# Optimization experiments

Hardware: AMD Instinct MI355X
Metric: run time of the kernel (lower is better)

The kernel has to match this reference:

```python
import jax, jax.numpy as jnp
import numpy as np

N, C, H, W = 16, 256, 48, 96
S = 64   # num_s = 2*num_state_mid; also num_n = mids*mids = 64 (must match)
EPS = 1e-5


def setup_inputs() -> dict:
    key = jax.random.key(0)
    ks = jax.random.split(key, 11)
    sc = 0.05
    return {
        "x": jax.random.normal(ks[0], (N, C, H, W), jnp.float32),
        "edge": jax.random.normal(ks[1], (N, 2, H, W), jnp.float32),
        # conv_state: Conv2d(C, S, 1) with bias
        "Ws": jax.random.normal(ks[2], (S, C), jnp.float32) * sc,
        "bs": jax.random.normal(ks[3], (S,), jnp.float32) * sc,
        # conv_proj: Conv2d(C, S, 1) with bias
        "Wp": jax.random.normal(ks[4], (S, C), jnp.float32) * sc,
        "bp": jax.random.normal(ks[5], (S,), jnp.float32) * sc,
        # GCN conv1: Conv1d(num_n, num_n, 1, bias=False)
        "W1": jax.random.normal(ks[6], (S, S), jnp.float32) * sc,
        # GCN conv2: Conv1d(S, S, 1, bias=False)
        "W2": jax.random.normal(ks[7], (S, S), jnp.float32) * sc,
        # conv_extend: Conv2d(S, C, 1, bias=False)
        "We": jax.random.normal(ks[8], (C, S), jnp.float32) * sc,
        # BatchNorm2d(C) affine params (training-mode batch stats used in forward)
        "gamma": jnp.ones((C,), jnp.float32),
        "beta": jnp.zeros((C,), jnp.float32),
    }


def reference(x, edge, Ws, bs, Wp, bp, W1, W2, We, gamma, beta):
    n, c, h, w = x.shape
    s = Ws.shape[0]
    # edge softmax over channels, take class-1 probability map  -> (n,1,h,w)
    edge_g = jax.nn.softmax(edge, axis=1)[:, 1:2]

    # 1x1 convs as channel matmuls
    xs = jnp.einsum('oc,nchw->nohw', Ws, x) + bs[None, :, None, None]
    xs = xs.reshape(n, s, h * w)                        # (n,S,HW)
    xp = jnp.einsum('oc,nchw->nohw', Wp, x) + bp[None, :, None, None]
    # x_proj_region + x_proj_edge == xp * (1 + edge_gate)
    comb = (xp * (1.0 + edge_g)).reshape(n, s, h * w)
    comb = jax.nn.softmax(comb, axis=-1)                # softmax over spatial

    # project to graph space: (n,S,HW) @ (n,HW,S) -> (n,S,S)
    xn = jnp.einsum('nsk,ntk->nst', xs, comb)

    # GCN: conv1 over node dim (last axis mixes via W1), subtract, conv2 over state dim, relu
    hh = jnp.einsum('ij,nsj->nsi', W1, xn) - xn
    hh = jax.nn.relu(jnp.einsum('ij,njk->nik', W2, hh))

    # back-project: (n,S,S) @ (n,S,HW) -> (n,S,HW) -> (n,S,H,W)
    xr = jnp.einsum('nst,ntk->nsk', hh, comb).reshape(n, s, h, w)

    # conv_extend (no bias) then BatchNorm2d in training mode (biased batch var)
    ext = jnp.einsum('os,nshw->nohw', We, xr)
    mean = ext.mean(axis=(0, 2, 3), keepdims=True)
    var = ext.var(axis=(0, 2, 3), keepdims=True)
    bn = gamma[None, :, None, None] * (ext - mean) * jax.lax.rsqrt(var + EPS) \
         + beta[None, :, None, None]
    return x + bn
```

## Files before the change

### kernel.cpp

```cpp
#include <hip/hip_runtime.h>

#define HW 4608
#define NB 16
#define CC 256
#define SS 64
#define EPS 1e-5f
#define NSPLIT 24

typedef __attribute__((ext_vector_type(8))) short short8;
typedef __attribute__((ext_vector_type(4))) float f32x4;

__device__ __forceinline__ ushort f2bf(float f) {
    uint u = __float_as_uint(f);
    return (ushort)((u + 0x7FFFu + ((u >> 16) & 1u)) >> 16);
}
__device__ __forceinline__ float bf2f(ushort h) {
    return __uint_as_float(((uint)h) << 16);
}

__global__ __launch_bounds__(256) void k_wf(const float* __restrict__ Ws,
                                            const float* __restrict__ Wp,
                                            ushort* __restrict__ Wf) {
    int idx = blockIdx.x * 256 + threadIdx.x;
    int j = idx & 7, r = (idx >> 3) & 127, kq = (idx >> 10) & 3, cs = idx >> 12;
    int c = cs * 32 + kq * 8 + j;
    float v = (r < 64) ? Ws[r * CC + c] : Wp[(r - 64) * CC + c];
    Wf[idx] = f2bf(v);
}

__global__ __launch_bounds__(256) void k_proj(const float* __restrict__ x,
                                              const ushort* __restrict__ Wf,
                                              const float* __restrict__ bs,
                                              const float* __restrict__ bp,
                                              const float* __restrict__ edge,
                                              ushort* __restrict__ xsb,
                                              ushort* __restrict__ Eb,
                                              float* __restrict__ rsum) {
    __shared__ __align__(16) ushort Bl[4 * 128 * 8];
    int n = blockIdx.y, k0 = blockIdx.x * 128;
    int tid = threadIdx.x, lane = tid & 63, w = tid >> 6;
    int wr = w >> 1, wn = w & 1;
    int q = lane >> 4, li = lane & 15;
    int sn = tid & 127, kq0 = (tid >> 7) * 2;
    f32x4 acc[4][4] = {};
    for (int cs = 0; cs < 8; cs++) {
#pragma unroll
        for (int kk = 0; kk < 2; kk++) {
            int kq = kq0 + kk;
            union { ushort u[8]; uint4 v; } tmp;
#pragma unroll
            for (int j = 0; j < 8; j++) {
                float vv = x[((size_t)n * CC + cs * 32 + kq * 8 + j) * HW + k0 + sn];
                tmp.u[j] = f2bf(vv);
            }
            *(uint4*)&Bl[(kq * 128 + sn) * 8] = tmp.v;
        }
        __syncthreads();
        short8 af[4], bfr[4];
#pragma unroll
        for (int m = 0; m < 4; m++) {
            int r = wr * 64 + m * 16 + li;
            uint4 t = *(const uint4*)&Wf[((cs * 4 + q) * 128 + r) * 8];
            af[m] = *(short8*)&t;
        }
#pragma unroll
        for (int nn = 0; nn < 4; nn++) {
            int nl = wn * 64 + nn * 16 + li;
            uint4 t = *(const uint4*)&Bl[(q * 128 + nl) * 8];
            bfr[nn] = *(short8*)&t;
        }
#pragma unroll
        for (int m = 0; m < 4; m++)
#pragma unroll
            for (int nn = 0; nn < 4; nn++)
                acc[m][nn] = __builtin_amdgcn_mfma_f32_16x16x32_bf16(af[m], bfr[nn], acc[m][nn], 0, 0, 0);
        __syncthreads();
    }
    if (wr == 0) {
#pragma unroll
        for (int m = 0; m < 4; m++) {
#pragma unroll
            for (int rr = 0; rr < 4; rr++) {
                int s = m * 16 + q * 4 + rr;
                float bv = bs[s];
#pragma unroll
                for (int nn = 0; nn < 4; nn++) {
                    int col = k0 + wn * 64 + nn * 16 + li;
                    xsb[((size_t)n * SS + s) * HW + col] = f2bf(acc[m][nn][rr] + bv);
                }
            }
        }
    } else {
        float ga[4];
#pragma unroll
        for (int nn = 0; nn < 4; nn++) {
            int col = k0 + wn * 64 + nn * 16 + li;
            float e0 = edge[((size_t)n * 2 + 0) * HW + col];
            float e1 = edge[((size_t)n * 2 + 1) * HW + col];
            ga[nn] = 1.f + 1.f / (1.f + __expf(e0 - e1));
        }
        float rp[4][4];
#pragma unroll
        for (int m = 0; m < 4; m++) {
#pragma unroll
            for (int rr = 0; rr < 4; rr++) {
                int s = m * 16 + q * 4 + rr;
                float bv = bp[s];
                float sum = 0.f;
#pragma unroll
                for (int nn = 0; nn < 4; nn++) {
                    int col = k0 + wn * 64 + nn * 16 + li;
                    float e = __expf((acc[m][nn][rr] + bv) * ga[nn]);
                    sum += e;
                    Eb[((size_t)n * SS + s) * HW + col] = f2bf(e);
                }
                rp[m][rr] = sum;
            }
        }
#pragma unroll
        for (int b = 1; b < 16; b <<= 1)
#pragma unroll
            for (int m = 0; m < 4; m++)
#pragma unroll
                for (int rr = 0; rr < 4; rr++)
                    rp[m][rr] += __shfl_xor(rp[m][rr], b, 64);
        if (li == 0) {
#pragma unroll
            for (int m = 0; m < 4; m++)
#pragma unroll
                for (int rr = 0; rr < 4; rr++)
                    atomicAdd(&rsum[n * SS + m * 16 + q * 4 + rr], rp[m][rr]);
        }
    }
}

__global__ __launch_bounds__(256) void k_graph(const ushort* __restrict__ xsb,
                                               const ushort* __restrict__ Eb,
                                               float* __restrict__ Up,
                                               float* __restrict__ Pp) {
    int n = blockIdx.y, sp = blockIdx.x;
    int kbase = sp * (HW / NSPLIT);
    int tid = threadIdx.x, lane = tid & 63, w = tid >> 6;
    int q = lane >> 4, li = lane & 15;
    bool isP = w >= 2;
    int half = w & 1;
    const ushort* Arow = isP ? Eb : xsb;
    f32x4 acc[2][4] = {};
    for (int ks = 0; ks < (HW / NSPLIT) / 32; ks++) {
        int kb = kbase + ks * 32 + q * 8;
        short8 af[2], bfr[4];
#pragma unroll
        for (int mt = 0; mt < 2; mt++) {
            int s = half * 32 + mt * 16 + li;
            uint4 t = *(const uint4*)&Arow[((size_t)n * SS + s) * HW + kb];
            af[mt] = *(short8*)&t;
        }
#pragma unroll
        for (int nt = 0; nt < 4; nt++) {
            int tt = nt * 16 + li;
            uint4 t = *(const uint4*)&Eb[((size_t)n * SS + tt) * HW + kb];
            bfr[nt] = *(short8*)&t;
        }
#pragma unroll
        for (int mt = 0; mt < 2; mt++)
#pragma unroll
            for (int nt = 0; nt < 4; nt++)
                acc[mt][nt] = __builtin_amdgcn_mfma_f32_16x16x32_bf16(af[mt], bfr[nt], acc[mt][nt], 0, 0, 0);
    }
    float* dst = (isP ? Pp : Up) + ((size_t)sp * NB + n) * 4096;
#pragma unroll
    for (int mt = 0; mt < 2; mt++)
#pragma unroll
        for (int nt = 0; nt < 4; nt++)
#pragma unroll
            for (int rr = 0; rr < 4; rr++) {
                int row = half * 32 + mt * 16 + q * 4 + rr;
                int col = nt * 16 + li;
                dst[row * 64 + col] = acc[mt][nt][rr];
            }
}

__global__ __launch_bounds__(256) void k_red(const float* __restrict__ Up,
                                             const float* __restrict__ Pp,
                                             float* __restrict__ U,
                                             float* __restrict__ P) {
    int idx = blockIdx.x * 256 + threadIdx.x;
    const float* src = (idx < 65536) ? Up : Pp;
    float* dst = (idx < 65536) ? U : P;
    int o = idx & 65535;
    float s = 0.f;
    for (int sp = 0; sp < NSPLIT; sp++) s += src[(size_t)sp * 65536 + o];
    dst[o] = s;
}

__global__ __launch_bounds__(256) void k_gcn(const float* __restrict__ U,
                                             const float* __restrict__ rsum,
                                             const float* __restrict__ W1,
                                             const float* __restrict__ W2,
                                             const float* __restrict__ We,
                                             float* __restrict__ M,
                                             ushort* __restrict__ Mf) {
    __shared__ __align__(16) float A[64 * 68];
    __shared__ __align__(16) float B[64 * 68];
    __shared__ __align__(16) float Cb[64 * 68];
    __shared__ float rs[64];
    int n = blockIdx.x;
    int cc = blockIdx.y;
    int tid = threadIdx.x;
    int t0 = tid >> 4, t1 = tid & 15;
    if (tid < 64) rs[tid] = 1.0f / rsum[n * SS + tid];
    __syncthreads();
#pragma unroll
    for (int i = 0; i < 16; i++) {
        int idx = tid + i * 256;
        int r = idx >> 6, cth = idx & 63;
        A[cth * 68 + r] = U[n * 4096 + idx] * rs[cth];
        B[cth * 68 + r] = W1[idx];
    }
    __syncthreads();
    {
        float acc[4][4] = {};
        for (int j = 0; j < 64; j++) {
            float4 a4 = *(const float4*)&A[j * 68 + t0 * 4];
            float4 b4 = *(const float4*)&B[j * 68 + t1 * 4];
            float a[4] = {a4.x, a4.y, a4.z, a4.w};
            float b[4] = {b4.x, b4.y, b4.z, b4.w};
#pragma unroll
            for (int p = 0; p < 4; p++)
#pragma unroll
                for (int qq = 0; qq < 4; qq++) acc[p][qq] += a[p] * b[qq];
        }
#pragma unroll
        for (int p = 0; p < 4; p++)
#pragma unroll
            for (int qq = 0; qq < 4; qq++) {
                acc[p][qq] -= A[(t1 * 4 + qq) * 68 + (t0 * 4 + p)];
                Cb[(t0 * 4 + p) * 68 + t1 * 4 + qq] = acc[p][qq];
            }
    }
    __syncthreads();
#pragma unroll
    for (int i = 0; i < 16; i++) {
        int idx = tid + i * 256;
        int r = idx >> 6, cth = idx & 63;
        B[cth * 68 + r] = W2[idx];
    }
    __syncthreads();
    {
        float acc[4][4] = {};
        for (int j = 0; j < 64; j++) {
            float4 a4 = *(const float4*)&B[j * 68 + t0 * 4];
            float4 b4 = *(const float4*)&Cb[j * 68 + t1 * 4];
            float a[4] = {a4.x, a4.y, a4.z, a4.w};
            float b[4] = {b4.x, b4.y, b4.z, b4.w};
#pragma unroll
            for (int p = 0; p < 4; p++)
#pragma unroll
                for (int qq = 0; qq < 4; qq++) acc[p][qq] += a[p] * b[qq];
        }
        __syncthreads();
#pragma unroll
        for (int p = 0; p < 4; p++)
#pragma unroll
            for (int qq = 0; qq < 4; qq++)
                A[(t0 * 4 + p) * 68 + t1 * 4 + qq] = fmaxf(acc[p][qq], 0.f);
    }
    __syncthreads();
#pragma unroll
    for (int i = 0; i < 16; i++) {
        int idx = tid + i * 256;
        int c = idx >> 6, j = idx & 63;
        B[j * 68 + c] = We[(cc * 64 + c) * 64 + j];
    }
    __syncthreads();
    {
        float acc[4][4] = {};
        for (int j = 0; j < 64; j++) {
            float4 a4 = *(const float4*)&B[j * 68 + t0 * 4];
            float4 b4 = *(const float4*)&A[j * 68 + t1 * 4];
            float a[4] = {a4.x, a4.y, a4.z, a4.w};
            float b[4] = {b4.x, b4.y, b4.z, b4.w};
#pragma unroll
            for (int p = 0; p < 4; p++)
#pragma unroll
                for (int qq = 0; qq < 4; qq++) acc[p][qq] += a[p] * b[qq];
        }
#pragma unroll
        for (int p = 0; p < 4; p++) {
            int c = cc * 64 + t0 * 4 + p;
            float v[4];
#pragma unroll
            for (int qq = 0; qq < 4; qq++) v[qq] = acc[p][qq] * rs[t1 * 4 + qq];
            float4 st = {v[0], v[1], v[2], v[3]};
            *(float4*)&M[((size_t)n * CC + c) * 64 + t1 * 4] = st;
#pragma unroll
            for (int qq = 0; qq < 4; qq++) {
                int t = t1 * 4 + qq;
                Mf[(size_t)n * 16384 + ((t >> 3) * 256 + c) * 8 + (t & 7)] = f2bf(v[qq]);
            }
        }
    }
}

__global__ __launch_bounds__(256) void k_stats(const float* __restrict__ M,
                                               const float* __restrict__ P,
                                               const float* __restrict__ rsum,
                                               const float* __restrict__ gamma,
                                               const float* __restrict__ beta,
                                               float* __restrict__ sc,
                                               float* __restrict__ bi) {
    __shared__ float ms[64];
    __shared__ float rst[64];
    __shared__ float red[256];
    int c = blockIdx.x;
    int tid = threadIdx.x;
    float qa = 0.f, sa = 0.f;
    for (int n = 0; n < NB; n++) {
        if (tid < 64) ms[tid] = M[((size_t)n * CC + c) * 64 + tid];
        else if (tid < 128) rst[tid - 64] = rsum[n * SS + tid - 64];
        __syncthreads();
#pragma unroll
        for (int p = 0; p < 16; p++) {
            int e = p * 256 + tid;
            qa += ms[e >> 6] * ms[e & 63] * P[n * 4096 + e];
        }
        if ((tid & 63) == 0) {
#pragma unroll
            for (int p = 0; p < 16; p++) {
                int s = (p * 256 + tid) >> 6;
                sa += ms[s] * rst[s];
            }
        }
        __syncthreads();
    }
    red[tid] = qa;
    __syncthreads();
    for (int off = 128; off > 0; off >>= 1) {
        if (tid < off) red[tid] += red[tid + off];
        __syncthreads();
    }
    float qtot = red[0];
    __syncthreads();
    red[tid] = sa;
    __syncthreads();
    for (int off = 128; off > 0; off >>= 1) {
        if (tid < off) red[tid] += red[tid + off];
        __syncthreads();
    }
    float stot = red[0];
    if (tid == 0) {
        const float invM = 1.0f / ((float)NB * (float)HW);
        float mean = stot * invM;
        float var = qtot * invM - mean * mean;
        float s = gamma[c] * rsqrtf(var + EPS);
        sc[c] = s;
        bi[c] = beta[c] - s * mean;
    }
}

__global__ __launch_bounds__(256) void k_out(const float* __restrict__ x,
                                             const ushort* __restrict__ Mf,
                                             const ushort* __restrict__ Eb,
                                             const float* __restrict__ sc,
                                             const float* __restrict__ bi,
                                             float* __restrict__ out) {
    __shared__ __align__(16) ushort Bl[8 * 64 * 8];
    int n = blockIdx.y, k0 = blockIdx.x * 64;
    int tid = threadIdx.x, lane = tid & 63, w = tid >> 6;
    int q = lane >> 4, li = lane & 15;
    {
        int nl = tid & 63, pr = tid >> 6;
#pragma unroll
        for (int kk = 0; kk < 2; kk++) {
            int kq = pr * 2 + kk;
            union { ushort u[8]; uint4 v; } tmp;
#pragma unroll
            for (int j = 0; j < 8; j++)
                tmp.u[j] = Eb[((size_t)n * SS + kq * 8 + j) * HW + k0 + nl];
            *(uint4*)&Bl[(kq * 64 + nl) * 8] = tmp.v;
        }
    }
    __syncthreads();
    f32x4 acc[4][4] = {};
#pragma unroll
    for (int ks = 0; ks < 2; ks++) {
        short8 af[4], bfr[4];
#pragma unroll
        for (int mt = 0; mt < 4; mt++) {
            int c = w * 64 + mt * 16 + li;
            uint4 t = *(const uint4*)&Mf[(size_t)n * 16384 + ((ks * 4 + q) * 256 + c) * 8];
            af[mt] = *(short8*)&t;
        }
#pragma unroll
        for (int nt = 0; nt < 4; nt++) {
            int nl = nt * 16 + li;
            uint4 t = *(const uint4*)&Bl[((ks * 4 + q) * 64 + nl) * 8];
            bfr[nt] = *(short8*)&t;
        }
#pragma unroll
        for (int mt = 0; mt < 4; mt++)
#pragma unroll
            for (int nt = 0; nt < 4; nt++)
                acc[mt][nt] = __builtin_amdgcn_mfma_f32_16x16x32_bf16(af[mt], bfr[nt], acc[mt][nt], 0, 0, 0);
    }
#pragma unroll
    for (int mt = 0; mt < 4; mt++) {
#pragma unroll
        for (int rr = 0; rr < 4; rr++) {
            int c = w * 64 + mt * 16 + q * 4 + rr;
            float s_ = sc[c], bv = bi[c];
            size_t base = ((size_t)n * CC + c) * HW + k0;
#pragma unroll
            for (int nt = 0; nt < 4; nt++) {
                int col = nt * 16 + li;
                out[base + col] = x[base + col] + s_ * acc[mt][nt][rr] + bv;
            }
        }
    }
}

extern "C" void kernel_launch(void* const* d_in, const int* in_sizes, int n_in,
                              void* d_out, int out_size, void* d_ws, size_t ws_size,
                              hipStream_t stream) {
    const float* x = (const float*)d_in[0];
    const float* edge = (const float*)d_in[1];
    const float* Ws = (const float*)d_in[2];
    const float* bs = (const float*)d_in[3];
    const float* Wp = (const float*)d_in[4];
    const float* bp = (const float*)d_in[5];
    const float* W1 = (const float*)d_in[6];
    const float* W2 = (const float*)d_in[7];
    const float* We = (const float*)d_in[8];
    const float* gamma = (const float*)d_in[9];
    const float* beta = (const float*)d_in[10];
    float* out = (float*)d_out;

    char* base = (char*)d_ws;
    ushort* Wf  = (ushort*)base;                    base += 65536;
    ushort* xsb = (ushort*)base;                    base += 9437184;
    ushort* Eb  = (ushort*)base;                    base += 9437184;
    float*  Up  = (float*)base;                     base += (size_t)NSPLIT * NB * 4096 * 4;
    float*  Pp  = (float*)base;                     base += (size_t)NSPLIT * NB * 4096 * 4;
    float*  U   = (float*)base;                     base += 262144;
    float*  P   = (float*)base;                     base += 262144;
    float*  rsum= (float*)base;                     base += 4096;
    float*  M   = (float*)base;                     base += 1048576;
    ushort* Mf  = (ushort*)base;                    base += 524288;
    float*  sc  = (float*)base;                     base += 1024;
    float*  bi  = (float*)base;                     base += 1024;

    hipMemsetAsync(rsum, 0, 1024 * sizeof(float), stream);
    k_wf<<<128, 256, 0, stream>>>(Ws, Wp, Wf);
    k_proj<<<dim3(36, NB), 256, 0, stream>>>(x, Wf, bs, bp, edge, xsb, Eb, rsum);
    k_graph<<<dim3(NSPLIT, NB), 256, 0, stream>>>(xsb, Eb, Up, Pp);
    k_red<<<512, 256, 0, stream>>>(Up, Pp, U, P);
    k_gcn<<<dim3(NB, 4), 256, 0, stream>>>(U, rsum, W1, W2, We, M, Mf);
    k_stats<<<256, 256, 0, stream>>>(M, P, rsum, gamma, beta, sc, bi);
    k_out<<<dim3(72, NB), 256, 0, stream>>>(x, Mf, Eb, sc, bi, out);
}
```

Before: 235.8 us.

## Register double-buffer loads in projection and graph kernels, drop LDS staging

k_proj now loads x straight from global into registers, one column per lane, instead of staging through shared memory with two barriers per step. The next channel slice and weight fragment are prefetched while the current MFMAs run. Tile width is halved to 64 columns so the grid doubles. k_graph gets the same register double-buffered prefetch, and k_out batches its x loads ahead of the stores. The trade-off is higher register pressure and column-strided global loads that may coalesce less well.

```diff
diff --git a/kernel.cpp b/kernel.cpp
--- a/kernel.cpp
+++ b/kernel.cpp
@@ -36,46 +36,59 @@
                                               ushort* __restrict__ xsb,
                                               ushort* __restrict__ Eb,
                                               float* __restrict__ rsum) {
-    __shared__ __align__(16) ushort Bl[4 * 128 * 8];
-    int n = blockIdx.y, k0 = blockIdx.x * 128;
+    int n = blockIdx.y, k0 = blockIdx.x * 64;
     int tid = threadIdx.x, lane = tid & 63, w = tid >> 6;
     int wr = w >> 1, wn = w & 1;
     int q = lane >> 4, li = lane & 15;
-    int sn = tid & 127, kq0 = (tid >> 7) * 2;
-    f32x4 acc[4][4] = {};
+    const float* xb = x + (size_t)n * CC * HW + k0 + wn * 32 + li;
+
+    float pfB[2][2][8];
+    short8 af[2][4];
+    f32x4 acc[4][2] = {};
+
+#pragma unroll
+    for (int nt = 0; nt < 2; nt++)
+#pragma unroll
+        for (int j = 0; j < 8; j++)
+            pfB[0][nt][j] = xb[(size_t)(q * 8 + j) * HW + nt * 16];
+#pragma unroll
+    for (int m = 0; m < 4; m++) {
+        int r = wr * 64 + m * 16 + li;
+        uint4 t = *(const uint4*)&Wf[((0 * 4 + q) * 128 + r) * 8];
+        af[0][m] = *(short8*)&t;
+    }
+
+#pragma unroll
     for (int cs = 0; cs < 8; cs++) {
-#pragma unroll
-        for (int kk = 0; kk < 2; kk++) {
-            int kq = kq0 + kk;
-            union { ushort u[8]; uint4 v; } tmp;
-#pragma unroll
-            for (int j = 0; j < 8; j++) {
-                float vv = x[((size_t)n * CC + cs * 32 + kq * 8 + j) * HW + k0 + sn];
-                tmp.u[j] = f2bf(vv);
-            }
-            *(uint4*)&Bl[(kq * 128 + sn) * 8] = tmp.v;
-        }
-        __syncthreads();
-        short8 af[4], bfr[4];
-#pragma unroll
-        for (int m = 0; m < 4; m++) {
-            int r = wr * 64 + m * 16 + li;
-            uint4 t = *(const uint4*)&Wf[((cs * 4 + q) * 128 + r) * 8];
-            af[m] = *(short8*)&t;
-        }
-#pragma unroll
-        for (int nn = 0; nn < 4; nn++) {
-            int nl = wn * 64 + nn * 16 + li;
-            uint4 t = *(const uint4*)&Bl[(q * 128 + nl) * 8];
-            bfr[nn] = *(short8*)&t;
+        int cur = cs & 1, nxt = cur ^ 1;
+        if (cs < 7) {
+#pragma unroll
+            for (int nt = 0; nt < 2; nt++)
+#pragma unroll
+                for (int j = 0; j < 8; j++)
+                    pfB[nxt][nt][j] = xb[(size_t)((cs + 1) * 32 + q * 8 + j) * HW + nt * 16];
+#pragma unroll
+            for (int m = 0; m < 4; m++) {
+                int r = wr * 64 + m * 16 + li;
+                uint4 t = *(const uint4*)&Wf[(((cs + 1) * 4 + q) * 128 + r) * 8];
+                af[nxt][m] = *(short8*)&t;
+            }
+        }
+        short8 bfr[2];
+#pragma unroll
+        for (int nt = 0; nt < 2; nt++) {
+            union { ushort u[8]; short8 s; } tmp;
+#pragma unroll
+            for (int j = 0; j < 8; j++) tmp.u[j] = f2bf(pfB[cur][nt][j]);
+            bfr[nt] = tmp.s;
         }
 #pragma unroll
         for (int m = 0; m < 4; m++)
 #pragma unroll
-            for (int nn = 0; nn < 4; nn++)
-                acc[m][nn] = __builtin_amdgcn_mfma_f32_16x16x32_bf16(af[m], bfr[nn], acc[m][nn], 0, 0, 0);
-        __syncthreads();
-    }
+            for (int nt = 0; nt < 2; nt++)
+                acc[m][nt] = __builtin_amdgcn_mfma_f32_16x16x32_bf16(af[cur][m], bfr[nt], acc[m][nt], 0, 0, 0);
+    }
+
     if (wr == 0) {
 #pragma unroll
         for (int m = 0; m < 4; m++) {
@@ -84,20 +97,20 @@
                 int s = m * 16 + q * 4 + rr;
                 float bv = bs[s];
 #pragma unroll
-                for (int nn = 0; nn < 4; nn++) {
-                    int col = k0 + wn * 64 + nn * 16 + li;
-                    xsb[((size_t)n * SS + s) * HW + col] = f2bf(acc[m][nn][rr] + bv);
+                for (int nt = 0; nt < 2; nt++) {
+                    int col = k0 + wn * 32 + nt * 16 + li;
+                    xsb[((size_t)n * SS + s) * HW + col] = f2bf(acc[m][nt][rr] + bv);
                 }
             }
         }
     } else {
-        float ga[4];
-#pragma unroll
-        for (int nn = 0; nn < 4; nn++) {
-            int col = k0 + wn * 64 + nn * 16 + li;
+        float ga[2];
+#pragma unroll
+        for (int nt = 0; nt < 2; nt++) {
+            int col = k0 + wn * 32 + nt * 16 + li;
             float e0 = edge[((size_t)n * 2 + 0) * HW + col];
             float e1 = edge[((size_t)n * 2 + 1) * HW + col];
-            ga[nn] = 1.f + 1.f / (1.f + __expf(e0 - e1));
+            ga[nt] = 1.f + 1.f / (1.f + __expf(e0 - e1));
         }
         float rp[4][4];
 #pragma unroll
@@ -108,9 +121,9 @@
                 float bv = bp[s];
                 float sum = 0.f;
 #pragma unroll
-                for (int nn = 0; nn < 4; nn++) {
-                    int col = k0 + wn * 64 + nn * 16 + li;
-                    float e = __expf((acc[m][nn][rr] + bv) * ga[nn]);
+                for (int nt = 0; nt < 2; nt++) {
+                    int col = k0 + wn * 32 + nt * 16 + li;
+                    float e = __expf((acc[m][nt][rr] + bv) * ga[nt]);
                     sum += e;
                     Eb[((size_t)n * SS + s) * HW + col] = f2bf(e);
                 }
@@ -145,27 +158,47 @@
     bool isP = w >= 2;
     int half = w & 1;
     const ushort* Arow = isP ? Eb : xsb;
+    const int NITER = (HW / NSPLIT) / 32;
     f32x4 acc[2][4] = {};
-    for (int ks = 0; ks < (HW / NSPLIT) / 32; ks++) {
-        int kb = kbase + ks * 32 + q * 8;
-        short8 af[2], bfr[4];
+    short8 af[2][2], bfr[2][4];
+    {
+        int kb = kbase + q * 8;
 #pragma unroll
         for (int mt = 0; mt < 2; mt++) {
             int s = half * 32 + mt * 16 + li;
             uint4 t = *(const uint4*)&Arow[((size_t)n * SS + s) * HW + kb];
-            af[mt] = *(short8*)&t;
+            af[0][mt] = *(short8*)&t;
         }
 #pragma unroll
         for (int nt = 0; nt < 4; nt++) {
             int tt = nt * 16 + li;
             uint4 t = *(const uint4*)&Eb[((size_t)n * SS + tt) * HW + kb];
-            bfr[nt] = *(short8*)&t;
+            bfr[0][nt] = *(short8*)&t;
+        }
+    }
+#pragma unroll
+    for (int ks = 0; ks < NITER; ks++) {
+        int cur = ks & 1, nxt = cur ^ 1;
+        if (ks < NITER - 1) {
+            int kb = kbase + (ks + 1) * 32 + q * 8;
+#pragma unroll
+            for (int mt = 0; mt < 2; mt++) {
+                int s = half * 32 + mt * 16 + li;
+                uint4 t = *(const uint4*)&Arow[((size_t)n * SS + s) * HW + kb];
+                af[nxt][mt] = *(short8*)&t;
+            }
+#pragma unroll
+            for (int nt = 0; nt < 4; nt++) {
+                int tt = nt * 16 + li;
+                uint4 t = *(const uint4*)&Eb[((size_t)n * SS + tt) * HW + kb];
+                bfr[nxt][nt] = *(short8*)&t;
+            }
         }
 #pragma unroll
         for (int mt = 0; mt < 2; mt++)
 #pragma unroll
             for (int nt = 0; nt < 4; nt++)
-                acc[mt][nt] = __builtin_amdgcn_mfma_f32_16x16x32_bf16(af[mt], bfr[nt], acc[mt][nt], 0, 0, 0);
+                acc[mt][nt] = __builtin_amdgcn_mfma_f32_16x16x32_bf16(af[cur][mt], bfr[cur][nt], acc[mt][nt], 0, 0, 0);
     }
     float* dst = (isP ? Pp : Up) + ((size_t)sp * NB + n) * 4096;
 #pragma unroll
@@ -405,6 +438,15 @@
     }
 #pragma unroll
     for (int mt = 0; mt < 4; mt++) {
+        float xv[4][4];
+#pragma unroll
+        for (int rr = 0; rr < 4; rr++) {
+            int c = w * 64 + mt * 16 + q * 4 + rr;
+            size_t base = ((size_t)n * CC + c) * HW + k0;
+#pragma unroll
+            for (int nt = 0; nt < 4; nt++)
+                xv[rr][nt] = x[base + nt * 16 + li];
+        }
 #pragma unroll
         for (int rr = 0; rr < 4; rr++) {
             int c = w * 64 + mt * 16 + q * 4 + rr;
@@ -413,7 +455,7 @@
 #pragma unroll
             for (int nt = 0; nt < 4; nt++) {
                 int col = nt * 16 + li;
-                out[base + col] = x[base + col] + s_ * acc[mt][nt][rr] + bv;
+                out[base + col] = xv[rr][nt] + s_ * acc[mt][nt][rr] + bv;
             }
         }
     }
@@ -451,7 +493,7 @@
 
     hipMemsetAsync(rsum, 0, 1024 * sizeof(float), stream);
     k_wf<<<128, 256, 0, stream>>>(Ws, Wp, Wf);
-    k_proj<<<dim3(36, NB), 256, 0, stream>>>(x, Wf, bs, bp, edge, xsb, Eb, rsum);
+    k_proj<<<dim3(72, NB), 256, 0, stream>>>(x, Wf, bs, bp, edge, xsb, Eb, rsum);
     k_graph<<<dim3(NSPLIT, NB), 256, 0, stream>>>(xsb, Eb, Up, Pp);
     k_red<<<512, 256, 0, stream>>>(Up, Pp, U, P);
     k_gcn<<<dim3(NB, 4), 256, 0, stream>>>(U, rsum, W1, W2, We, M, Mf);
```

Result: slower. 245.6 us (+4.2%).
